# Kernel optimization log

Hardware: AMD Instinct MI355X
Metric: run time of the kernel (lower is better)

## Reference

```python
import jax, jax.numpy as jnp
import numpy as np

WINSIZE = 11
SIGMA = 1.5
L_RANGE = 1.0

def _gaussian_window(winsize, channel, dtype=jnp.float32):
    x = jnp.arange(winsize, dtype=dtype)
    g = jnp.exp(-((x - winsize // 2) ** 2) / (2.0 * SIGMA ** 2))
    g = g / g.sum()
    w2d = jnp.outer(g, g)                      # [ws, ws]
    # depthwise kernel [channel, 1, ws, ws] (OIHW, feature_group_count=channel)
    return jnp.broadcast_to(w2d, (channel, 1, winsize, winsize))

def _dwconv(x, w, channel):
    pad = WINSIZE // 2
    return jax.lax.conv_general_dilated(
        x, w, window_strides=(1, 1), padding=[(pad, pad), (pad, pad)],
        dimension_numbers=('NCHW', 'OIHW', 'NCHW'),
        feature_group_count=channel)

def _ssim(X, Y):
    channel = X.shape[1]
    w = _gaussian_window(WINSIZE, channel, X.dtype)
    mu1 = _dwconv(X, w, channel)
    mu2 = _dwconv(Y, w, channel)
    mu1_sq = mu1 * mu1
    mu2_sq = mu2 * mu2
    mu1_mu2 = mu1 * mu2
    sigma1_sq = _dwconv(X * X, w, channel) - mu1_sq
    sigma2_sq = _dwconv(Y * Y, w, channel) - mu2_sq
    sigma12 = _dwconv(X * Y, w, channel) - mu1_mu2
    C1 = (0.01 * L_RANGE) ** 2
    C2 = (0.03 * L_RANGE) ** 2
    ssim_map = ((2.0 * mu1_mu2 + C1) * (2.0 * sigma12 + C2)) / \
               ((mu1_sq + mu2_sq + C1) * (sigma1_sq + sigma2_sq + C2))
    return jnp.mean(ssim_map)  # sizeavg=True

def setup_inputs() -> dict:
    key = jax.random.key(0)
    k1, k2 = jax.random.split(key)
    shape = (16, 3, 512, 512)
    X = jax.random.uniform(k1, shape, dtype=jnp.float32)
    Y = jax.random.uniform(k2, shape, dtype=jnp.float32)
    return {"X": X, "Y": Y}

def reference(X, Y):
    return 1.0 - _ssim(X, Y)
```

## Files before the change

kernel.cpp:

```cpp
#include <hip/hip_runtime.h>


#define ROWS 32
#define COLS 256
#define NI   (ROWS + 10)
#define LW   (COLS + 10)
#define NIMG 48
#define NBLOCKS (NIMG * 2 * 16)
#define NPIXEL 12582912.0

__global__ __launch_bounds__(256) void ssim_row_kernel(
    const float* __restrict__ X, const float* __restrict__ Y,
    float* __restrict__ partial)
{
    __shared__ float sb[2][2][LW + 6];

    const int tid = threadIdx.x;
    const int bid = blockIdx.x;
    const int img = bid >> 5;
    const int rem = bid & 31;
    const int c0  = (rem & 1) * COLS;
    const int r0  = (rem >> 1) * ROWS;

    const float* __restrict__ Xi = X + (size_t)img * (512 * 512);
    const float* __restrict__ Yi = Y + (size_t)img * (512 * 512);

    float g[11];
    {
        float s = 0.f;
        #pragma unroll
        for (int i = 0; i < 11; ++i) {
            float d = (float)(i - 5);
            float e = expf(-d * d * (1.0f / 4.5f));
            g[i] = e; s += e;
        }
        float inv = 1.0f / s;
        #pragma unroll
        for (int i = 0; i < 11; ++i) g[i] *= inv;
    }

    const bool tail = (tid < LW - COLS);
    const int  gc0  = c0 - 5 + tid;
    const int  gc1  = gc0 + COLS;

    {
        int gr = r0 - 5;
        float x0 = 0.f, y0 = 0.f, x1 = 0.f, y1 = 0.f;
        if ((unsigned)gr < 512u) {
            const float* xr = Xi + (size_t)gr * 512;
            const float* yr = Yi + (size_t)gr * 512;
            if ((unsigned)gc0 < 512u) { x0 = xr[gc0]; y0 = yr[gc0]; }
            if (tail && (unsigned)gc1 < 512u) { x1 = xr[gc1]; y1 = yr[gc1]; }
        }
        sb[0][0][tid] = x0; sb[0][1][tid] = y0;
        if (tail) { sb[0][0][tid + COLS] = x1; sb[0][1][tid + COLS] = y1; }
    }
    __syncthreads();

    float ring[5][11];
    float acc = 0.f;

    const float C1 = 1e-4f, C2 = 9e-4f;

    #pragma unroll 1
    for (int jb = 0; jb < 44; jb += 11) {
        #pragma unroll
        for (int ph = 0; ph < 11; ++ph) {
            int j = jb + ph;
            if (j < NI) {
                const int cur = j & 1, nxt = cur ^ 1;
                const int jn = j + 1;

                float nx0 = 0.f, ny0 = 0.f, nx1 = 0.f, ny1 = 0.f;
                if (jn < NI) {
                    int gr = r0 - 5 + jn;
                    if ((unsigned)gr < 512u) {
                        const float* xr = Xi + (size_t)gr * 512;
                        const float* yr = Yi + (size_t)gr * 512;
                        if ((unsigned)gc0 < 512u) { nx0 = xr[gc0]; ny0 = yr[gc0]; }
                        if (tail && (unsigned)gc1 < 512u) { nx1 = xr[gc1]; ny1 = yr[gc1]; }
                    }
                }

                {
                    float hx = 0.f, hy = 0.f, hxx = 0.f, hyy = 0.f, hxy = 0.f;
                    #pragma unroll
                    for (int k = 0; k < 11; ++k) {
                        float x = sb[cur][0][tid + k];
                        float y = sb[cur][1][tid + k];
                        float w = g[k];
                        float wx = w * x, wy = w * y;
                        hx += wx; hy += wy;
                        hxx = fmaf(wx, x, hxx);
                        hyy = fmaf(wy, y, hyy);
                        hxy = fmaf(wx, y, hxy);
                    }
                    ring[0][ph] = hx;  ring[1][ph] = hy;
                    ring[2][ph] = hxx; ring[3][ph] = hyy; ring[4][ph] = hxy;
                }

                if (j >= 10) {
                    float mu1 = 0.f, mu2 = 0.f, vxx = 0.f, vyy = 0.f, vxy = 0.f;
                    #pragma unroll
                    for (int k = 0; k < 11; ++k) {
                        const int s = (ph + 1 + k) % 11;
                        float w = g[k];
                        mu1 = fmaf(w, ring[0][s], mu1);
                        mu2 = fmaf(w, ring[1][s], mu2);
                        vxx = fmaf(w, ring[2][s], vxx);
                        vyy = fmaf(w, ring[3][s], vyy);
                        vxy = fmaf(w, ring[4][s], vxy);
                    }
                    float m11 = mu1 * mu1, m22 = mu2 * mu2, m12 = mu1 * mu2;
                    float s1 = vxx - m11, s2 = vyy - m22, s12 = vxy - m12;
                    float num = (2.f * m12 + C1) * (2.f * s12 + C2);
                    float den = (m11 + m22 + C1) * (s1 + s2 + C2);
                    acc = fmaf(num, __builtin_amdgcn_rcpf(den), acc);
                }

                if (jn < NI) {
                    sb[nxt][0][tid] = nx0; sb[nxt][1][tid] = ny0;
                    if (tail) { sb[nxt][0][tid + COLS] = nx1; sb[nxt][1][tid + COLS] = ny1; }
                }
                __syncthreads();
            }
        }
    }

    #pragma unroll
    for (int off = 32; off > 0; off >>= 1)
        acc += __shfl_down(acc, off, 64);

    __shared__ float wsum[4];
    const int lane = tid & 63, wid = tid >> 6;
    if (lane == 0) wsum[wid] = acc;
    __syncthreads();
    if (tid == 0)
        partial[bid] = wsum[0] + wsum[1] + wsum[2] + wsum[3];
}

__global__ __launch_bounds__(256) void ssim_reduce_kernel(
    const float* __restrict__ partial, float* __restrict__ out)
{
    const int tid = threadIdx.x;
    double s = 0.0;
    for (int i = tid; i < NBLOCKS; i += 256) s += (double)partial[i];
    __shared__ double sd[256];
    sd[tid] = s;
    __syncthreads();
    for (int off = 128; off > 0; off >>= 1) {
        if (tid < off) sd[tid] += sd[tid + off];
        __syncthreads();
    }
    if (tid == 0) out[0] = (float)(1.0 - sd[0] / NPIXEL);
}

extern "C" void kernel_launch(void* const* d_in, const int* in_sizes, int n_in,
                              void* d_out, int out_size, void* d_ws, size_t ws_size,
                              hipStream_t stream) {
    const float* X = (const float*)d_in[0];
    const float* Y = (const float*)d_in[1];
    float* partial = (float*)d_ws;
    float* out = (float*)d_out;

    ssim_row_kernel<<<NBLOCKS, 256, 0, stream>>>(X, Y, partial);
    ssim_reduce_kernel<<<1, 256, 0, stream>>>(partial, out);
}
```

Baseline: 70.84 us.

## Pack two output columns per thread using half2 arithmetic for the SSIM convolutions

Moves the separable Gaussian convolutions to packed fp16 (__half2), with each thread computing two adjacent columns. Each block now covers a full 512-wide row strip instead of half of one, so the block count is halved. Shared memory stores even- and odd-shifted half2 copies so the packed operands stay aligned. This targets ALU throughput and removes the horizontal halo overlap, but fp16 accumulation of the squared and cross terms risks precision loss in the variance subtraction.

```diff
diff --git a/kernel.cpp b/kernel.cpp
--- a/kernel.cpp
+++ b/kernel.cpp
@@ -1,26 +1,22 @@
 #include <hip/hip_runtime.h>
+#include <hip/hip_fp16.h>
 
 
 #define ROWS 32
-#define COLS 256
 #define NI   (ROWS + 10)
-#define LW   (COLS + 10)
-#define NIMG 48
-#define NBLOCKS (NIMG * 2 * 16)
+#define NBLOCKS (48 * 16)
 #define NPIXEL 12582912.0
 
-__global__ __launch_bounds__(256) void ssim_row_kernel(
+__global__ __launch_bounds__(256) void ssim_pk_kernel(
     const float* __restrict__ X, const float* __restrict__ Y,
     float* __restrict__ partial)
 {
-    __shared__ float sb[2][2][LW + 6];
+    __shared__ __half2 sb[2][2][2][262];
 
     const int tid = threadIdx.x;
     const int bid = blockIdx.x;
-    const int img = bid >> 5;
-    const int rem = bid & 31;
-    const int c0  = (rem & 1) * COLS;
-    const int r0  = (rem >> 1) * ROWS;
+    const int img = bid >> 4;
+    const int r0  = (bid & 15) * ROWS;
 
     const float* __restrict__ Xi = X + (size_t)img * (512 * 512);
     const float* __restrict__ Yi = Y + (size_t)img * (512 * 512);
@@ -38,28 +34,50 @@
         #pragma unroll
         for (int i = 0; i < 11; ++i) g[i] *= inv;
     }
-
-    const bool tail = (tid < LW - COLS);
-    const int  gc0  = c0 - 5 + tid;
-    const int  gc1  = gc0 + COLS;
+    __half2 w2[11];
+    #pragma unroll
+    for (int i = 0; i < 11; ++i) w2[i] = __float2half2_rn(g[i]);
+
+    const __half2 hz = __float2half2_rn(0.f);
+
+    if (tid < 2) {
+        #pragma unroll
+        for (int b = 0; b < 2; ++b)
+            #pragma unroll
+            for (int m = 0; m < 2; ++m) {
+                sb[b][m][0][1 + tid]   = hz;
+                sb[b][m][0][259 + tid] = hz;
+                sb[b][m][1][tid]       = hz;
+                sb[b][m][1][259 + tid] = hz;
+            }
+    }
+
+    const int c2 = 2 * tid;
 
     {
         int gr = r0 - 5;
-        float x0 = 0.f, y0 = 0.f, x1 = 0.f, y1 = 0.f;
+        float2 xv = {0.f, 0.f}, yv = {0.f, 0.f};
+        float xn = 0.f, yn = 0.f;
         if ((unsigned)gr < 512u) {
             const float* xr = Xi + (size_t)gr * 512;
             const float* yr = Yi + (size_t)gr * 512;
-            if ((unsigned)gc0 < 512u) { x0 = xr[gc0]; y0 = yr[gc0]; }
-            if (tail && (unsigned)gc1 < 512u) { x1 = xr[gc1]; y1 = yr[gc1]; }
-        }
-        sb[0][0][tid] = x0; sb[0][1][tid] = y0;
-        if (tail) { sb[0][0][tid + COLS] = x1; sb[0][1][tid + COLS] = y1; }
+            xv = *(const float2*)(xr + c2);
+            yv = *(const float2*)(yr + c2);
+            if (tid < 255) { xn = xr[c2 + 2]; yn = yr[c2 + 2]; }
+        }
+        sb[0][0][0][tid + 3] = __floats2half2_rn(xv.x, xv.y);
+        sb[0][0][1][tid + 3] = __floats2half2_rn(xv.y, xn);
+        sb[0][1][0][tid + 3] = __floats2half2_rn(yv.x, yv.y);
+        sb[0][1][1][tid + 3] = __floats2half2_rn(yv.y, yn);
+        if (tid == 0) {
+            sb[0][0][1][2] = __floats2half2_rn(0.f, xv.x);
+            sb[0][1][1][2] = __floats2half2_rn(0.f, yv.x);
+        }
     }
     __syncthreads();
 
-    float ring[5][11];
+    __half2 ring[5][11];
     float acc = 0.f;
-
     const float C1 = 1e-4f, C2 = 9e-4f;
 
     #pragma unroll 1
@@ -71,56 +89,81 @@
                 const int cur = j & 1, nxt = cur ^ 1;
                 const int jn = j + 1;
 
-                float nx0 = 0.f, ny0 = 0.f, nx1 = 0.f, ny1 = 0.f;
+                float2 nxv = {0.f, 0.f}, nyv = {0.f, 0.f};
+                float nxn = 0.f, nyn = 0.f;
                 if (jn < NI) {
                     int gr = r0 - 5 + jn;
                     if ((unsigned)gr < 512u) {
                         const float* xr = Xi + (size_t)gr * 512;
                         const float* yr = Yi + (size_t)gr * 512;
-                        if ((unsigned)gc0 < 512u) { nx0 = xr[gc0]; ny0 = yr[gc0]; }
-                        if (tail && (unsigned)gc1 < 512u) { nx1 = xr[gc1]; ny1 = yr[gc1]; }
+                        nxv = *(const float2*)(xr + c2);
+                        nyv = *(const float2*)(yr + c2);
+                        if (tid < 255) { nxn = xr[c2 + 2]; nyn = yr[c2 + 2]; }
                     }
                 }
 
                 {
-                    float hx = 0.f, hy = 0.f, hxx = 0.f, hyy = 0.f, hxy = 0.f;
+                    const __half2* ex = &sb[cur][0][0][tid];
+                    const __half2* ox = &sb[cur][0][1][tid];
+                    const __half2* ey = &sb[cur][1][0][tid];
+                    const __half2* oy = &sb[cur][1][1][tid];
+                    __half2 hx = hz, hy = hz, hxx = hz, hyy = hz, hxy = hz;
                     #pragma unroll
                     for (int k = 0; k < 11; ++k) {
-                        float x = sb[cur][0][tid + k];
-                        float y = sb[cur][1][tid + k];
-                        float w = g[k];
-                        float wx = w * x, wy = w * y;
-                        hx += wx; hy += wy;
-                        hxx = fmaf(wx, x, hxx);
-                        hyy = fmaf(wy, y, hyy);
-                        hxy = fmaf(wx, y, hxy);
+                        __half2 xk = (k & 1) ? ex[(k + 1) >> 1] : ox[k >> 1];
+                        __half2 yk = (k & 1) ? ey[(k + 1) >> 1] : oy[k >> 1];
+                        __half2 wx = __hmul2(w2[k], xk);
+                        __half2 wy = __hmul2(w2[k], yk);
+                        hx  = __hadd2(hx, wx);
+                        hy  = __hadd2(hy, wy);
+                        hxx = __hfma2(wx, xk, hxx);
+                        hyy = __hfma2(wy, yk, hyy);
+                        hxy = __hfma2(wx, yk, hxy);
                     }
                     ring[0][ph] = hx;  ring[1][ph] = hy;
                     ring[2][ph] = hxx; ring[3][ph] = hyy; ring[4][ph] = hxy;
                 }
 
                 if (j >= 10) {
-                    float mu1 = 0.f, mu2 = 0.f, vxx = 0.f, vyy = 0.f, vxy = 0.f;
+                    __half2 mu1 = hz, mu2 = hz, vxx = hz, vyy = hz, vxy = hz;
                     #pragma unroll
                     for (int k = 0; k < 11; ++k) {
                         const int s = (ph + 1 + k) % 11;
-                        float w = g[k];
-                        mu1 = fmaf(w, ring[0][s], mu1);
-                        mu2 = fmaf(w, ring[1][s], mu2);
-                        vxx = fmaf(w, ring[2][s], vxx);
-                        vyy = fmaf(w, ring[3][s], vyy);
-                        vxy = fmaf(w, ring[4][s], vxy);
-                    }
-                    float m11 = mu1 * mu1, m22 = mu2 * mu2, m12 = mu1 * mu2;
-                    float s1 = vxx - m11, s2 = vyy - m22, s12 = vxy - m12;
-                    float num = (2.f * m12 + C1) * (2.f * s12 + C2);
-                    float den = (m11 + m22 + C1) * (s1 + s2 + C2);
-                    acc = fmaf(num, __builtin_amdgcn_rcpf(den), acc);
+                        mu1 = __hfma2(w2[k], ring[0][s], mu1);
+                        mu2 = __hfma2(w2[k], ring[1][s], mu2);
+                        vxx = __hfma2(w2[k], ring[2][s], vxx);
+                        vyy = __hfma2(w2[k], ring[3][s], vyy);
+                        vxy = __hfma2(w2[k], ring[4][s], vxy);
+                    }
+                    float2 m1 = __half22float2(mu1);
+                    float2 m2 = __half22float2(mu2);
+                    float2 xx = __half22float2(vxx);
+                    float2 yy = __half22float2(vyy);
+                    float2 xy = __half22float2(vxy);
+                    #pragma unroll
+                    for (int h = 0; h < 2; ++h) {
+                        float a1 = h ? m1.y : m1.x;
+                        float a2 = h ? m2.y : m2.x;
+                        float bx = h ? xx.y : xx.x;
+                        float by = h ? yy.y : yy.x;
+                        float bz = h ? xy.y : xy.x;
+                        float m11 = a1 * a1, m22 = a2 * a2, m12 = a1 * a2;
+                        float s1 = bx - m11, s2 = by - m22, s12 = bz - m12;
+                        float num = (2.f * m12 + C1) * (2.f * s12 + C2);
+                        float den = (m11 + m22 + C1) * (s1 + s2 + C2);
+                        acc = fmaf(num, __builtin_amdgcn_rcpf(den), acc);
+                    }
                 }
 
                 if (jn < NI) {
-                    sb[nxt][0][tid] = nx0; sb[nxt][1][tid] = ny0;
-                    if (tail) { sb[nxt][0][tid + COLS] = nx1; sb[nxt][1][tid + COLS] = ny1; }
+                    sb[nxt][0][0][tid + 3] = __floats2half2_rn(nxv.x, nxv.y);
+                    sb[nxt][0][1][tid + 3] = __floats2half2_rn(nxv.y, nxn);
+                    sb[nxt][1][0][tid + 3] = __floats2half2_rn(nyv.x, nyv.y);
+                    sb[nxt][1][1][tid + 3] = __floats2half2_rn(nyv.y, nyn);
+                    if (tid == 0) {
+                        sb[nxt][0][1][2] = __floats2half2_rn(0.f, nxv.x);
+                        sb[nxt][1][1][2] = __floats2half2_rn(0.f, nyv.x);
+                    }
                 }
                 __syncthreads();
             }
@@ -163,6 +206,6 @@
     float* partial = (float*)d_ws;
     float* out = (float*)d_out;
 
-    ssim_row_kernel<<<NBLOCKS, 256, 0, stream>>>(X, Y, partial);
+    ssim_pk_kernel<<<NBLOCKS, 256, 0, stream>>>(X, Y, partial);
     ssim_reduce_kernel<<<1, 256, 0, stream>>>(partial, out);
 }
```

After: 63.82 us. 1.11x faster.
